# Kernel tuning notes

Hardware: AMD Instinct MI355X
Metric: run time of the kernel (lower is better)

## Reference

```python
import jax, jax.numpy as jnp
import numpy as np

HEADS = 12
KEY_DIM = 16
B, C, H, W = 16, 384, 64, 64


def _hard_swish(x):
    return x * jnp.clip(x + 3.0, 0.0, 6.0) / 6.0


def _affine(x, g, b):
    # Inference-mode BatchNorm folded into per-channel scale/shift (NCHW).
    return x * g[:, None, None] + b[:, None, None]


def _pw(x, w):
    # 1x1 conv as a channel contraction: x [B,Cin,H,W], w [Cout,Cin].
    return jnp.einsum('bchw,oc->bohw', x, w)


def setup_inputs() -> dict:
    key = jax.random.key(0)
    ks = jax.random.split(key, 20)
    d = {}
    d['x'] = jax.random.normal(ks[0], (B, C, H, W), dtype=jnp.float32)
    d['rnd_offset'] = jax.random.uniform(ks[1], (B, 2, 1, 1), dtype=jnp.float32) * 6.0 - 3.0
    S = HEADS * KEY_DIM  # 192
    d['proj_w'] = jax.random.normal(ks[2], (3 * S, C + 2), dtype=jnp.float32) * 0.05
    d['proj_g'] = jax.random.uniform(ks[3], (3 * S,), dtype=jnp.float32) + 0.5
    d['proj_b'] = jax.random.normal(ks[4], (3 * S,), dtype=jnp.float32) * 0.1
    d['vp2_w'] = jax.random.normal(ks[5], (C, S), dtype=jnp.float32) * 0.05
    d['vp2_g'] = jax.random.uniform(ks[6], (C,), dtype=jnp.float32) + 0.5
    d['vp2_b'] = jax.random.normal(ks[7], (C,), dtype=jnp.float32) * 0.1
    d['dw_w'] = jax.random.normal(ks[8], (C, 1, 5, 5), dtype=jnp.float32) * 0.1
    d['dw_g'] = jax.random.uniform(ks[9], (C,), dtype=jnp.float32) + 0.5
    d['dw_b'] = jax.random.normal(ks[10], (C,), dtype=jnp.float32) * 0.1
    d['pw1_w'] = jax.random.normal(ks[11], (4 * C, C), dtype=jnp.float32) * 0.05
    d['pw1_g'] = jax.random.uniform(ks[12], (4 * C,), dtype=jnp.float32) + 0.5
    d['pw1_b'] = jax.random.normal(ks[13], (4 * C,), dtype=jnp.float32) * 0.1
    d['pw2_w'] = jax.random.normal(ks[14], (C, 4 * C), dtype=jnp.float32) * 0.05
    d['out_g'] = jax.random.uniform(ks[15], (C,), dtype=jnp.float32) + 0.5
    d['out_b'] = jax.random.normal(ks[16], (C,), dtype=jnp.float32) * 0.1
    d['rz_attn'] = jnp.float32(0.1)
    d['rz_ffn'] = jnp.float32(0.1)
    d['embed_strength'] = jnp.float32(-10.0)
    return d


def reference(x, rnd_offset, proj_w, proj_g, proj_b, vp2_w, vp2_g, vp2_b,
              dw_w, dw_g, dw_b, pw1_w, pw1_g, pw1_b, pw2_w, out_g, out_b,
              rz_attn, rz_ffn, embed_strength):
    b, c, h, w = x.shape
    # --- learned-strength positional embedding with random per-image offset ---
    xp = jnp.arange(w, dtype=x.dtype) / 1000.0
    yp = jnp.arange(h, dtype=x.dtype) / 1000.0
    xx, yy = jnp.meshgrid(xp, yp, indexing='xy')      # each (H, W)
    pos = jnp.stack([xx, yy], axis=0)[None]           # (1, 2, H, W)
    pos = jnp.exp(embed_strength) * (pos + rnd_offset)  # (B, 2, H, W)
    x_emb = jnp.concatenate([x, pos], axis=1)         # (B, C+2, H, W)

    # --- qkv projection (1x1 conv + BN + ReLU), computed in fp32 ---
    proj = jax.nn.relu(_affine(_pw(x_emb, proj_w), proj_g, proj_b))
    proj = proj.astype(jnp.float32)

    S = HEADS * KEY_DIM
    N = h * w

    def get_slice(i):
        # (B, S, H, W) slice -> (B*heads, N, key_dim)
        s = proj[:, i * S:(i + 1) * S]
        return s.reshape(b * HEADS, KEY_DIM, N).transpose(0, 2, 1)

    q, k, v = get_slice(0), get_slice(1), get_slice(2)

    # --- non-causal linear attention: Q (K^T V) / (Q sum(K)) ---
    ktv = jnp.einsum('bnd,bne->bde', k, v)            # (B*heads, d, d)
    numer = jnp.einsum('bnd,bde->bne', q, ktv)        # (B*heads, N, d)
    denom = jnp.einsum('bnd,bd->bn', q, k.sum(axis=1))[..., None]  # (B*heads, N, 1)
    out = numer / jnp.maximum(denom, 1e-4)
    out = out.transpose(0, 2, 1).reshape(b, S, h, w)  # (B, heads*key_dim, H, W)

    # --- value projection back to channels ---
    out = jax.nn.relu(_affine(_pw(out, vp2_w), vp2_g, vp2_b))
    y = x + rz_attn * out

    # --- FFN: depthwise 5x5 -> expand 1x1 -> project 1x1 (+ BNs) ---
    z = jax.lax.conv_general_dilated(
        y, dw_w, window_strides=(1, 1), padding='SAME',
        dimension_numbers=('NCHW', 'OIHW', 'NCHW'), feature_group_count=c)
    z = _hard_swish(_affine(z, dw_g, dw_b))
    z = _hard_swish(_affine(_pw(z, pw1_w), pw1_g, pw1_b))
    z = _affine(_pw(z, pw2_w), out_g, out_b)
    return y + rz_ffn * z
```

## Files before the change

### kernel.cpp

```cpp
#include <hip/hip_runtime.h>
#include <cstdint>

typedef unsigned short u16;
typedef __attribute__((ext_vector_type(8))) __bf16 bf16x8;
typedef __attribute__((ext_vector_type(4))) float f32x4;

__device__ __forceinline__ u16 f2bf(float f) {
    union { float f; uint32_t u; } v; v.f = f;
    uint32_t u = v.u;
    uint32_t r = (u + 0x7fffu + ((u >> 16) & 1u)) >> 16;
    return (u16)r;
}
__device__ __forceinline__ float bf2f(u16 h) {
    union { uint32_t u; float f; } v; v.u = ((uint32_t)h) << 16;
    return v.f;
}
__device__ __forceinline__ float bflo(uint32_t u) {
    union { uint32_t u; float f; } v; v.u = u << 16;
    return v.f;
}
__device__ __forceinline__ float bfhi(uint32_t u) {
    union { uint32_t u; float f; } v; v.u = u & 0xffff0000u;
    return v.f;
}

__device__ __forceinline__ void ld_lds16(const u16* g, u16* l) {
    __builtin_amdgcn_global_load_lds(
        (const __attribute__((address_space(1))) uint32_t*)g,
        (__attribute__((address_space(3))) uint32_t*)l, 16, 0, 0);
}

__global__ __launch_bounds__(256) void prep(
    const float* __restrict__ proj_w, const float* __restrict__ proj_g,
    const float* __restrict__ proj_b, const float* __restrict__ vp2_w,
    const float* __restrict__ pw1_w, const float* __restrict__ pw2_w,
    const float* __restrict__ dw_w,
    u16* __restrict__ w1p, u16* __restrict__ w2, u16* __restrict__ w3,
    u16* __restrict__ w4, float* __restrict__ gp, float2* __restrict__ dwp)
{
    int i = blockIdx.x * 256 + threadIdx.x;
    if (i < 245760) {
        int o = i / 384, k = i - o * 384;
        w1p[i] = (o < 576) ? f2bf(proj_w[o * 386 + k]) : (u16)0;
        return;
    }
    i -= 245760;
    if (i < 73728) { w2[i] = f2bf(vp2_w[i]); return; }
    i -= 73728;
    if (i < 589824) { w3[i] = f2bf(pw1_w[i]); return; }
    i -= 589824;
    if (i < 589824) { w4[i] = f2bf(pw2_w[i]); return; }
    i -= 589824;
    if (i < 2560) {
        int which = i / 640, o = i - which * 640;
        float v = 0.f;
        if (o < 576) {
            v = (which == 0) ? proj_g[o] : (which == 1) ? proj_b[o]
                : (which == 2) ? proj_w[o * 386 + 384] : proj_w[o * 386 + 385];
        }
        gp[i] = v; return;
    }
    i -= 2560;
    if (i < 4800) {
        int tap = i / 192, cp = i - tap * 192;
        dwp[i] = make_float2(dw_w[(2 * cp) * 25 + tap], dw_w[(2 * cp + 1) * 25 + tap]);
    }
}

__global__ __launch_bounds__(256) void transpose_x(const float* __restrict__ x,
                                                   u16* __restrict__ xt)
{
    __shared__ float tile[64][65];
    int b = blockIdx.x, n0 = blockIdx.y * 64, c0 = blockIdx.z * 64;
    int t = threadIdx.x;
    int jj = t & 63, i0 = t >> 6;
    #pragma unroll
    for (int r = 0; r < 16; r++) {
        int ci = r * 4 + i0;
        tile[ci][jj] = x[((size_t)b * 384 + c0 + ci) * 4096 + n0 + jj];
    }
    __syncthreads();
    #pragma unroll
    for (int r = 0; r < 16; r++) {
        int ni = r * 4 + i0;
        xt[(size_t)(b * 4096 + n0 + ni) * 384 + c0 + jj] = f2bf(tile[jj][ni]);
    }
}

template <int MODE, int IM, int JN, int OUTT>
__global__ __launch_bounds__(256) void gemm_nhwc(
    const u16* __restrict__ A, const u16* __restrict__ W,
    u16* __restrict__ out, int K, int Osz, int nOT,
    const float* __restrict__ g, const float* __restrict__ bb,
    const float* __restrict__ w1x, const float* __restrict__ w1y,
    const u16* __restrict__ res, const float* __restrict__ sc,
    const float* __restrict__ rnd)
{
    constexpr int BK = 32;
    constexpr int BM = IM * 32;
    constexpr int BN = JN * 32;
    constexpr int GA = IM / 2;
    constexpr int GB = JN / 2;
    constexpr bool LEGACY = (IM == 4 && JN == 4);
    constexpr bool SPB = (JN >= IM);
    constexpr int NBUF = LEGACY ? 3 : 2;
    constexpr int NP1 = LEGACY ? 0 : (SPB ? GB / 2 : GA / 2);
    constexpr int NP0 = LEGACY ? 0 : (GA + GB - NP1);
    __shared__ __align__(16) u16 smem[NBUF * (BM + BN) * BK];

    const int tid = threadIdx.x;
    const int lane = tid & 63;
    const int wv = tid >> 6;
    const int wm = (wv >> 1) * (IM * 16);
    const int wn = (wv & 1) * (JN * 16);

    const int nwg = gridDim.x;
    const int q8 = nwg >> 3;
    const int b1 = (blockIdx.x & 7) * q8 + (blockIdx.x >> 3);
    const int mt = b1 / nOT;
    const int ot = b1 - mt * nOT;
    const int m0 = mt * BM;
    const int o0 = ot * BN;

    const int q = lane >> 4;
    const int mr = lane & 15;
    const int ks = (q ^ ((mr >> 1) & 3)) * 8;

    const int tq = tid >> 2;
    const int sl = tid & 3;
    const int tk = (sl ^ ((tq >> 1) & 3)) * 8;

    size_t ga[GA], gb[GB];
    int la[GA], lb[GB];
    #pragma unroll
    for (int gi = 0; gi < GA; gi++) {
        ga[gi] = (size_t)(m0 + gi * 64 + tq) * K + tk;
        la[gi] = (gi * 64 + tq) * BK + sl * 8;
    }
    #pragma unroll
    for (int gi = 0; gi < GB; gi++) {
        gb[gi] = (size_t)(o0 + gi * 64 + tq) * K + tk;
        lb[gi] = (gi * 64 + tq) * BK + sl * 8;
    }

    auto stage_all = [&](int tile, int bufi) {
        const size_t ko = (size_t)tile * BK;
        u16* sAb = smem + bufi * (BM * BK);
        u16* sBb = smem + NBUF * (BM * BK) + bufi * (BN * BK);
        #pragma unroll
        for (int gi = 0; gi < GA; gi++) ld_lds16(A + ga[gi] + ko, sAb + la[gi]);
        #pragma unroll
        for (int gi = 0; gi < GB; gi++) ld_lds16(W + gb[gi] + ko, sBb + lb[gi]);
    };
    auto stage_s0 = [&](int tile, int bufi) {
        const size_t ko = (size_t)tile * BK;
        u16* sAb = smem + bufi * (BM * BK);
        u16* sBb = smem + NBUF * (BM * BK) + bufi * (BN * BK);
        if constexpr (SPB) {
            #pragma unroll
            for (int gi = 0; gi < GA; gi++) ld_lds16(A + ga[gi] + ko, sAb + la[gi]);
            #pragma unroll
            for (int gi = 0; gi < GB; gi += 2) ld_lds16(W + gb[gi] + ko, sBb + lb[gi]);
        } else {
            #pragma unroll
            for (int gi = 0; gi < GA; gi += 2) ld_lds16(A + ga[gi] + ko, sAb + la[gi]);
            #pragma unroll
            for (int gi = 0; gi < GB; gi++) ld_lds16(W + gb[gi] + ko, sBb + lb[gi]);
        }
    };
    auto stage_s1 = [&](int tile, int bufi) {
        const size_t ko = (size_t)tile * BK;
        u16* sAb = smem + bufi * (BM * BK);
        u16* sBb = smem + NBUF * (BM * BK) + bufi * (BN * BK);
        if constexpr (SPB) {
            #pragma unroll
            for (int gi = 1; gi < GB; gi += 2) ld_lds16(W + gb[gi] + ko, sBb + lb[gi]);
        } else {
            #pragma unroll
            for (int gi = 1; gi < GA; gi += 2) ld_lds16(A + ga[gi] + ko, sAb + la[gi]);
        }
    };

    f32x4 acc[IM][JN] = {};
    const int nIter = K >> 5;
    int buf = 0;

    if constexpr (LEGACY) {
        stage_all(0, 0);
        if (nIter > 1) stage_all(1, 1);
        for (int t = 0; t < nIter; ++t) {
            if (t + 1 < nIter) asm volatile("s_waitcnt vmcnt(4)" ::: "memory");
            else               asm volatile("s_waitcnt vmcnt(0)" ::: "memory");
            __builtin_amdgcn_s_barrier();
            __builtin_amdgcn_sched_barrier(0);
            if (t + 2 < nIter) {
                int nb = buf + 2; if (nb >= 3) nb -= 3;
                stage_all(t + 2, nb);
            }
            const u16* sAr = smem + buf * (BM * BK);
            const u16* sBr = smem + NBUF * (BM * BK) + buf * (BN * BK);
            bf16x8 af[IM], bfr[JN];
            #pragma unroll
            for (int i = 0; i < IM; i++)
                af[i] = *(const bf16x8*)&sAr[(wm + i * 16 + mr) * BK + ks];
            #pragma unroll
            for (int j = 0; j < JN; j++)
                bfr[j] = *(const bf16x8*)&sBr[(wn + j * 16 + mr) * BK + ks];
            __builtin_amdgcn_s_setprio(1);
            #pragma unroll
            for (int i = 0; i < IM; i++)
                #pragma unroll
                for (int j = 0; j < JN; j++)
                    acc[i][j] = __builtin_amdgcn_mfma_f32_16x16x32_bf16(af[i], bfr[j], acc[i][j], 0, 0, 0);
            __builtin_amdgcn_s_setprio(0);
            buf++; if (buf == 3) buf = 0;
        }
    } else {
        stage_s0(0, 0);
        stage_s1(0, 0);
        for (int t = 0; t < nIter; ++t) {
            const u16* sAr = smem + buf * (BM * BK);
            const u16* sBr = smem + NBUF * (BM * BK) + buf * (BN * BK);
            bf16x8 af[IM], bfr[JN];
            asm volatile("s_waitcnt vmcnt(%0)" ::"i"(NP1) : "memory");
            __builtin_amdgcn_s_barrier();
            __builtin_amdgcn_sched_barrier(0);
            if constexpr (SPB) {
                #pragma unroll
                for (int i = 0; i < IM; i++)
                    af[i] = *(const bf16x8*)&sAr[(wm + i * 16 + mr) * BK + ks];
                #pragma unroll
                for (int j = 0; j < JN / 2; j++)
                    bfr[j] = *(const bf16x8*)&sBr[(wn + j * 16 + mr) * BK + ks];
            } else {
                #pragma unroll
                for (int i = 0; i < IM / 2; i++)
                    af[i] = *(const bf16x8*)&sAr[(wm + i * 16 + mr) * BK + ks];
                #pragma unroll
                for (int j = 0; j < JN; j++)
                    bfr[j] = *(const bf16x8*)&sBr[(wn + j * 16 + mr) * BK + ks];
            }
            if (t + 1 < nIter) stage_s0(t + 1, buf ^ 1);
            __builtin_amdgcn_s_setprio(1);
            if constexpr (SPB) {
                #pragma unroll
                for (int i = 0; i < IM; i++)
                    #pragma unroll
                    for (int j = 0; j < JN / 2; j++)
                        acc[i][j] = __builtin_amdgcn_mfma_f32_16x16x32_bf16(af[i], bfr[j], acc[i][j], 0, 0, 0);
            } else {
                #pragma unroll
                for (int i = 0; i < IM / 2; i++)
                    #pragma unroll
                    for (int j = 0; j < JN; j++)
                        acc[i][j] = __builtin_amdgcn_mfma_f32_16x16x32_bf16(af[i], bfr[j], acc[i][j], 0, 0, 0);
            }
            __builtin_amdgcn_s_setprio(0);
            if (t + 1 < nIter)
                asm volatile("s_waitcnt vmcnt(%0)" ::"i"(NP0) : "memory");
            else
                asm volatile("s_waitcnt vmcnt(0)" ::: "memory");
            __builtin_amdgcn_s_barrier();
            __builtin_amdgcn_sched_barrier(0);
            if constexpr (SPB) {
                #pragma unroll
                for (int j = JN / 2; j < JN; j++)
                    bfr[j] = *(const bf16x8*)&sBr[(wn + j * 16 + mr) * BK + ks];
            } else {
                #pragma unroll
                for (int i = IM / 2; i < IM; i++)
                    af[i] = *(const bf16x8*)&sAr[(wm + i * 16 + mr) * BK + ks];
            }
            if (t + 1 < nIter) stage_s1(t + 1, buf ^ 1);
            __builtin_amdgcn_s_setprio(1);
            if constexpr (SPB) {
                #pragma unroll
                for (int i = 0; i < IM; i++)
                    #pragma unroll
                    for (int j = JN / 2; j < JN; j++)
                        acc[i][j] = __builtin_amdgcn_mfma_f32_16x16x32_bf16(af[i], bfr[j], acc[i][j], 0, 0, 0);
            } else {
                #pragma unroll
                for (int i = IM / 2; i < IM; i++)
                    #pragma unroll
                    for (int j = 0; j < JN; j++)
                        acc[i][j] = __builtin_amdgcn_mfma_f32_16x16x32_bf16(af[i], bfr[j], acc[i][j], 0, 0, 0);
            }
            __builtin_amdgcn_s_setprio(0);
            buf ^= 1;
        }
    }

    float* st = (float*)smem;
    constexpr int LDE = BN + 4;
    constexpr int P = BM / 32;
    constexpr int HP = IM / 2;
    constexpr int NG = BN / 128;
    const int row_l = tid >> 3;
    const int cs16 = (tid & 7) * 16;

    float E = 0.f, offx = 0.f, offy = 0.f, rz = 0.f;
    if constexpr (MODE == 1) {
        E = expf(sc[0]);
        int bimg = m0 >> 12;
        offx = rnd[bimg * 2 + 0];
        offy = rnd[bimg * 2 + 1];
    }
    if constexpr (MODE == 2 || MODE == 4) rz = sc[0];

    float gv[NG][16], bv[NG][16];
    #pragma unroll
    for (int gg = 0; gg < NG; gg++)
        #pragma unroll
        for (int c = 0; c < 4; c++) {
            *(float4*)&gv[gg][c * 4] = *(const float4*)(g + o0 + gg * 128 + cs16 + c * 4);
            *(float4*)&bv[gg][c * 4] = *(const float4*)(bb + o0 + gg * 128 + cs16 + c * 4);
        }
    float wxv[16], wyv[16];
    if constexpr (MODE == 1) {
        #pragma unroll
        for (int c = 0; c < 4; c++) {
            *(float4*)&wxv[c * 4] = *(const float4*)(w1x + o0 + cs16 + c * 4);
            *(float4*)&wyv[c * 4] = *(const float4*)(w1y + o0 + cs16 + c * 4);
        }
    }

    #pragma unroll
    for (int p = 0; p < P; ++p) {
        __syncthreads();
        if ((wv >> 1) == p / HP) {
            const int ib = (p % HP) * 2;
            #pragma unroll
            for (int ii = 0; ii < 2; ++ii)
                #pragma unroll
                for (int j = 0; j < JN; ++j)
                    #pragma unroll
                    for (int r = 0; r < 4; ++r)
                        st[(ii * 16 + q * 4 + r) * LDE + wn + j * 16 + mr] =
                            acc[ib + ii][j][r];
        }
        __syncthreads();
        const int pix = m0 + p * 32 + row_l;
        float px = 0.f, py = 0.f;
        if constexpr (MODE == 1) {
            int n = pix & 4095;
            px = E * ((float)(n & 63) * 0.001f + offx);
            py = E * ((float)(n >> 6) * 0.001f + offy);
        }
        #pragma unroll
        for (int gg = 0; gg < NG; ++gg) {
            const int ob = o0 + gg * 128 + cs16;
            float vals[16];
            #pragma unroll
            for (int c = 0; c < 4; ++c)
                *(f32x4*)&vals[c * 4] =
                    *(const f32x4*)&st[row_l * LDE + gg * 128 + cs16 + c * 4];
            u16 rv[16];
            if constexpr (MODE == 2 || MODE == 4) {
                #pragma unroll
                for (int c = 0; c < 2; c++)
                    *(float4*)&rv[c * 8] = *(const float4*)(res + (size_t)pix * 384 + ob + c * 8);
            }
            float fv[16];
            #pragma unroll
            for (int e = 0; e < 16; ++e) {
                float v = vals[e];
                if constexpr (MODE == 1) {
                    v += px * wxv[e] + py * wyv[e];
                    v = fmaxf(gv[gg][e] * v + bv[gg][e], 0.f);
                } else if constexpr (MODE == 2) {
                    v = fmaxf(gv[gg][e] * v + bv[gg][e], 0.f);
                    v = bf2f(rv[e]) + rz * v;
                } else if constexpr (MODE == 3) {
                    float tv = gv[gg][e] * v + bv[gg][e];
                    v = tv * fminf(fmaxf(tv + 3.f, 0.f), 6.f) * (1.f / 6.f);
                } else {
                    float tv = gv[gg][e] * v + bv[gg][e];
                    v = bf2f(rv[e]) + rz * tv;
                }
                fv[e] = v;
            }
            if constexpr (OUTT) {
                #pragma unroll
                for (int c = 0; c < 4; ++c)
                    *(f32x4*)&st[row_l * LDE + gg * 128 + cs16 + c * 4] =
                        *(const f32x4*)&fv[c * 4];
            } else {
                u16 ov[16];
                #pragma unroll
                for (int e = 0; e < 16; ++e) ov[e] = f2bf(fv[e]);
                #pragma unroll
                for (int c = 0; c < 2; c++)
                    *(float4*)(out + (size_t)pix * Osz + ob + c * 8) = *(const float4*)&ov[c * 8];
            }
        }
        if constexpr (OUTT) {
            __syncthreads();
            const int cl = tid & 127;
            const int rh = tid >> 7;
            const int pixb = m0 + p * 32;
            const int bimg2 = pixb >> 12;
            const int n0 = (pixb & 4095) + rh * 16;
            float tv[16];
            #pragma unroll
            for (int k2 = 0; k2 < 16; ++k2)
                tv[k2] = st[(rh * 16 + k2) * LDE + cl];
            float* dst = (float*)out + ((size_t)bimg2 * 384 + o0 + cl) * 4096 + n0;
            #pragma unroll
            for (int c = 0; c < 4; c++)
                *(float4*)(dst + c * 4) = *(const float4*)&tv[c * 4];
        }
    }
}

__global__ __launch_bounds__(256) void attn_ktv(const u16* __restrict__ proj,
                                                float* __restrict__ ktvp)
{
    constexpr int LDT = 264;
    __shared__ u16 kt_[16 * LDT];
    __shared__ u16 vt_[16 * LDT];
    int bh = blockIdx.x;
    int ch = blockIdx.y;
    int b = bh / 12, h = bh - b * 12;
    const u16* base = proj + (size_t)b * 4096 * 640;
    int kc = 192 + h * 16, vc = 384 + h * 16;
    int t = threadIdx.x;
    int d = t >> 4, e = t & 15;
    float acc = 0.f, ksum = 0.f;
    for (int n0 = ch * 1024; n0 < ch * 1024 + 1024; n0 += 256) {
        __syncthreads();
        const u16* r = base + (size_t)(n0 + t) * 640;
        u16 kv[16], vv[16];
        *(float4*)&kv[0] = ((const float4*)(r + kc))[0];
        *(float4*)&kv[8] = ((const float4*)(r + kc))[1];
        *(float4*)&vv[0] = ((const float4*)(r + vc))[0];
        *(float4*)&vv[8] = ((const float4*)(r + vc))[1];
        #pragma unroll
        for (int dd = 0; dd < 16; dd++) {
            kt_[dd * LDT + t] = kv[dd];
            vt_[dd * LDT + t] = vv[dd];
        }
        __syncthreads();
        const u16* kr = &kt_[d * LDT];
        const u16* vr = &vt_[e * LDT];
        #pragma unroll 4
        for (int n = 0; n < 256; n += 8) {
            uint4 kw = *(const uint4*)(kr + n);
            uint4 vw = *(const uint4*)(vr + n);
            acc += bflo(kw.x) * bflo(vw.x) + bfhi(kw.x) * bfhi(vw.x);
            acc += bflo(kw.y) * bflo(vw.y) + bfhi(kw.y) * bfhi(vw.y);
            acc += bflo(kw.z) * bflo(vw.z) + bfhi(kw.z) * bfhi(vw.z);
            acc += bflo(kw.w) * bflo(vw.w) + bfhi(kw.w) * bfhi(vw.w);
        }
        if (t < 16) {
            const u16* krs = &kt_[t * LDT];
            #pragma unroll 4
            for (int n = 0; n < 256; n += 8) {
                uint4 kw = *(const uint4*)(krs + n);
                ksum += bflo(kw.x) + bfhi(kw.x) + bflo(kw.y) + bfhi(kw.y)
                      + bflo(kw.z) + bfhi(kw.z) + bflo(kw.w) + bfhi(kw.w);
            }
        }
    }
    float* o = ktvp + ((size_t)bh * 4 + ch) * 272;
    o[t] = acc;
    if (t < 16) o[256 + t] = ksum;
}

__global__ __launch_bounds__(256) void attn_apply(const u16* __restrict__ proj,
                                                  const float* __restrict__ ktvp,
                                                  u16* __restrict__ att)
{
    int bh = blockIdx.x;
    int b = bh / 12, h = bh - b * 12;
    __shared__ float kt[272];
    int t = threadIdx.x;
    {
        const float* p = ktvp + (size_t)bh * 4 * 272;
        kt[t] = p[t] + p[272 + t] + p[544 + t] + p[816 + t];
        if (t < 16) {
            int u = 256 + t;
            kt[u] = p[u] + p[272 + u] + p[544 + u] + p[816 + u];
        }
    }
    __syncthreads();
    int n = blockIdx.y * 256 + t;
    const u16* qr = proj + (size_t)(b * 4096 + n) * 640 + h * 16;
    u16 qb[16];
    *(float4*)&qb[0] = ((const float4*)qr)[0];
    *(float4*)&qb[8] = ((const float4*)qr)[1];
    float qv[16];
    #pragma unroll
    for (int d = 0; d < 16; d++) qv[d] = bf2f(qb[d]);
    float denom = 0.f;
    #pragma unroll
    for (int d = 0; d < 16; d++) denom += qv[d] * kt[256 + d];
    float rcp = 1.f / fmaxf(denom, 1e-4f);
    u16* op = att + (size_t)(b * 4096 + n) * 192 + h * 16;
    u16 ov[16];
    #pragma unroll
    for (int e = 0; e < 16; e++) {
        float s = 0.f;
        #pragma unroll
        for (int d = 0; d < 16; d++) s += qv[d] * kt[d * 16 + e];
        ov[e] = f2bf(s * rcp);
    }
    ((float4*)op)[0] = *(const float4*)&ov[0];
    ((float4*)op)[1] = *(const float4*)&ov[8];
}

__global__ __launch_bounds__(192) void dwconv(const u16* __restrict__ y,
                                              const float2* __restrict__ wt,
                                              const float* __restrict__ g,
                                              const float* __restrict__ bc,
                                              u16* __restrict__ z)
{
    const int cp = threadIdx.x;
    const int xc = blockIdx.x;
    const int b  = blockIdx.y;
    const int c0 = cp * 2;

    float2 wv[25];
    #pragma unroll
    for (int t = 0; t < 25; t++) wv[t] = wt[t * 192 + cp];
    const float g0 = g[c0], g1 = g[c0 + 1];
    const float b0 = bc[c0], b1 = bc[c0 + 1];

    const size_t ibase = (size_t)b * 4096;
    const u16* ycol = y + ibase * 384 + c0;

    uint32_t r0[5], r1[5], r2[5], r3[5], r4[5];

#define LOADROW(yy, dst)                                                     \
    {                                                                        \
        if ((unsigned)(yy) < 64u) {                                          \
            const u16* rp = ycol + (size_t)(yy) * 64 * 384;                  \
            _Pragma("unroll")                                                \
            for (int dx = 0; dx < 5; dx++) {                                 \
                int xx = xc + dx - 2;                                        \
                dst[dx] = ((unsigned)xx < 64u)                               \
                              ? *(const uint32_t*)(rp + (size_t)xx * 384)    \
                              : 0u;                                          \
            }                                                                \
        } else {                                                             \
            _Pragma("unroll")                                                \
            for (int dx = 0; dx < 5; dx++) dst[dx] = 0u;                     \
        }                                                                    \
    }

#define COMPUTE(yr, A, B, C, D, E)                                           \
    if ((yr) < 64) {                                                         \
        float a0 = 0.f, a1 = 0.f;                                            \
        _Pragma("unroll")                                                    \
        for (int dx = 0; dx < 5; dx++) {                                     \
            uint32_t p;                                                      \
            p = A[dx];                                                       \
            a0 += wv[dx].x * bf2f((u16)(p & 0xffffu));                       \
            a1 += wv[dx].y * bf2f((u16)(p >> 16));                           \
            p = B[dx];                                                       \
            a0 += wv[5 + dx].x * bf2f((u16)(p & 0xffffu));                   \
            a1 += wv[5 + dx].y * bf2f((u16)(p >> 16));                       \
            p = C[dx];                                                       \
            a0 += wv[10 + dx].x * bf2f((u16)(p & 0xffffu));                  \
            a1 += wv[10 + dx].y * bf2f((u16)(p >> 16));                      \
            p = D[dx];                                                       \
            a0 += wv[15 + dx].x * bf2f((u16)(p & 0xffffu));                  \
            a1 += wv[15 + dx].y * bf2f((u16)(p >> 16));                      \
            p = E[dx];                                                       \
            a0 += wv[20 + dx].x * bf2f((u16)(p & 0xffffu));                  \
            a1 += wv[20 + dx].y * bf2f((u16)(p >> 16));                      \
        }                                                                    \
        float t0 = g0 * a0 + b0;                                             \
        float t1 = g1 * a1 + b1;                                             \
        t0 = t0 * fminf(fmaxf(t0 + 3.f, 0.f), 6.f) * (1.f / 6.f);            \
        t1 = t1 * fminf(fmaxf(t1 + 3.f, 0.f), 6.f) * (1.f / 6.f);            \
        uint32_t packed = (uint32_t)f2bf(t0) | ((uint32_t)f2bf(t1) << 16);   \
        *(uint32_t*)(z + (ibase + (size_t)(yr) * 64 + xc) * 384 + c0) = packed; \
    }

#define STEP(yr, A, B, C, D, E)                                              \
    COMPUTE(yr, A, B, C, D, E)                                               \
    LOADROW((yr) + 3, A)

    LOADROW(-2, r0)
    LOADROW(-1, r1)
    LOADROW(0, r2)
    LOADROW(1, r3)
    LOADROW(2, r4)

    for (int base = 0; base < 65; base += 5) {
        STEP(base + 0, r0, r1, r2, r3, r4)
        STEP(base + 1, r1, r2, r3, r4, r0)
        STEP(base + 2, r2, r3, r4, r0, r1)
        STEP(base + 3, r3, r4, r0, r1, r2)
        STEP(base + 4, r4, r0, r1, r2, r3)
    }
#undef STEP
#undef COMPUTE
#undef LOADROW
}

extern "C" void kernel_launch(void* const* d_in, const int* in_sizes, int n_in,
                              void* d_out, int out_size, void* d_ws, size_t ws_size,
                              hipStream_t stream)
{
    (void)in_sizes; (void)n_in; (void)out_size; (void)ws_size;
    const float* x       = (const float*)d_in[0];
    const float* rnd     = (const float*)d_in[1];
    const float* proj_w  = (const float*)d_in[2];
    const float* proj_g  = (const float*)d_in[3];
    const float* proj_b  = (const float*)d_in[4];
    const float* vp2_w   = (const float*)d_in[5];
    const float* vp2_g   = (const float*)d_in[6];
    const float* vp2_b   = (const float*)d_in[7];
    const float* dw_w    = (const float*)d_in[8];
    const float* dw_g    = (const float*)d_in[9];
    const float* dw_b    = (const float*)d_in[10];
    const float* pw1_w   = (const float*)d_in[11];
    const float* pw1_g   = (const float*)d_in[12];
    const float* pw1_b   = (const float*)d_in[13];
    const float* pw2_w   = (const float*)d_in[14];
    const float* out_g   = (const float*)d_in[15];
    const float* out_b   = (const float*)d_in[16];
    const float* rz_attn = (const float*)d_in[17];
    const float* rz_ffn  = (const float*)d_in[18];
    const float* es      = (const float*)d_in[19];
    float* out = (float*)d_out;

    char* ws = (char*)d_ws;
    u16*   xt   = (u16*)(ws + 0);
    u16*   att  = (u16*)(ws + 50331648);
    u16*   z2   = (u16*)(ws + 0);
    u16*   proj = (u16*)(ws + 201326592);
    u16*   z1   = proj;
    u16*   yt   = (u16*)(ws + 285212672);
    u16*   w1p  = (u16*)(ws + 335753216);
    u16*   w2   = (u16*)(ws + 336244736);
    u16*   w3   = (u16*)(ws + 336392192);
    u16*   w4   = (u16*)(ws + 337571840);
    float* gp   = (float*)(ws + 338751488);
    float2* dwp = (float2*)(ws + 338761728);
    float* ktvp = (float*)(ws + 338800128);

    prep<<<5885, 256, 0, stream>>>(proj_w, proj_g, proj_b, vp2_w, pw1_w, pw2_w,
                                   dw_w, w1p, w2, w3, w4, gp, dwp);
    transpose_x<<<dim3(16, 64, 6), 256, 0, stream>>>(x, xt);
    gemm_nhwc<1, 4, 4, 0><<<2560, 256, 0, stream>>>(xt, w1p, proj, 384, 640, 5,
        gp, gp + 640, gp + 1280, gp + 1920, nullptr, es, rnd);
    attn_ktv<<<dim3(192, 4), 256, 0, stream>>>(proj, ktvp);
    attn_apply<<<dim3(192, 16), 256, 0, stream>>>(proj, ktvp, att);
    gemm_nhwc<2, 8, 4, 0><<<768, 256, 0, stream>>>(att, w2, yt, 192, 384, 3,
        vp2_g, vp2_b, nullptr, nullptr, xt, rz_attn, nullptr);
    dwconv<<<dim3(64, 16), 192, 0, stream>>>(yt, dwp, dw_g, dw_b, z1);
    gemm_nhwc<3, 4, 8, 0><<<3072, 256, 0, stream>>>(z1, w3, z2, 384, 1536, 6,
        pw1_g, pw1_b, nullptr, nullptr, nullptr, nullptr, nullptr);
    gemm_nhwc<4, 8, 4, 1><<<768, 256, 0, stream>>>(z2, w4, (u16*)out, 1536, 384, 3,
        out_g, out_b, nullptr, nullptr, yt, rz_ffn, nullptr);
}
```

Before: 666.4 us.

## Fuse FFN expand and project GEMMs into one kernel keeping hidden tile on-chip

Replaces the two FFN pointwise GEMM launches with a single kernel. Each 64-pixel block computes the 1536-wide hidden activation in 256-column chunks, applies BN and hard-swish, stages the chunk in LDS, and immediately accumulates it into the 384-channel output. This removes the round trip of the large z2 intermediate through HBM. In exchange the block holds 24 accumulator vectors in registers, uses about 94KB of LDS, and has fewer blocks per CU, which may lower occupancy.

```diff
diff --git a/kernel.cpp b/kernel.cpp
--- a/kernel.cpp
+++ b/kernel.cpp
@@ -406,6 +406,215 @@
             for (int k2 = 0; k2 < 16; ++k2)
                 tv[k2] = st[(rh * 16 + k2) * LDE + cl];
             float* dst = (float*)out + ((size_t)bimg2 * 384 + o0 + cl) * 4096 + n0;
+            #pragma unroll
+            for (int c = 0; c < 4; c++)
+                *(float4*)(dst + c * 4) = *(const float4*)&tv[c * 4];
+        }
+    }
+}
+
+__global__ __launch_bounds__(256) void ffn_fused(
+    const u16* __restrict__ z1, const u16* __restrict__ W3,
+    const u16* __restrict__ W4, const u16* __restrict__ res,
+    const float* __restrict__ g1, const float* __restrict__ b1f,
+    const float* __restrict__ g2, const float* __restrict__ b2f,
+    const float* __restrict__ sc, float* __restrict__ outp)
+{
+    __shared__ __align__(16) u16 smem[47104];
+    u16* sA = smem;
+    u16* sB = smem + 6144;
+    u16* sS = smem + 30720;
+
+    const int tid = threadIdx.x;
+    const int lane = tid & 63, wv = tid >> 6;
+    const int q = lane >> 4, mr = lane & 15;
+    const int wm1 = (wv >> 1) * 32;
+    const int wn1 = (wv & 1) * 128;
+    const int ks = (q ^ ((mr >> 1) & 3)) * 8;
+
+    const int nwg = gridDim.x;
+    const int q8 = nwg >> 3;
+    const int bsw = (blockIdx.x & 7) * q8 + (blockIdx.x >> 3);
+    const int m0 = bsw * 64;
+
+    const int tq = tid >> 2, sl = tid & 3;
+    const int tk = (sl ^ ((tq >> 1) & 3)) * 8;
+    const int loA = tid * 8;
+
+    const size_t gaA = (size_t)(m0 + tq) * 384 + tk;
+
+    const int R2 = wv * 16 + mr;
+    const int sbz = (q ^ ((R2 >> 1) & 3)) * 8;
+
+    f32x4 acc2[24] = {};
+
+    for (int ot = 0; ot < 6; ++ot) {
+        f32x4 acc1[2][8] = {};
+        const size_t w3b = (size_t)(ot * 256 + tq) * 384 + tk;
+        ld_lds16(z1 + gaA, sA + loA);
+        #pragma unroll
+        for (int gi = 0; gi < 4; gi++)
+            ld_lds16(W3 + w3b + (size_t)gi * 24576, sB + gi * 2048 + loA);
+        ld_lds16(z1 + gaA + 32, sA + 2048 + loA);
+        #pragma unroll
+        for (int gi = 0; gi < 4; gi++)
+            ld_lds16(W3 + w3b + 32 + (size_t)gi * 24576, sB + 8192 + gi * 2048 + loA);
+        int buf = 0;
+        for (int t = 0; t < 12; ++t) {
+            if (t < 11) asm volatile("s_waitcnt vmcnt(5)" ::: "memory");
+            else        asm volatile("s_waitcnt vmcnt(0)" ::: "memory");
+            __builtin_amdgcn_s_barrier();
+            __builtin_amdgcn_sched_barrier(0);
+            if (t + 2 < 12) {
+                int nb = buf + 2; if (nb >= 3) nb -= 3;
+                const int ko = (t + 2) * 32;
+                ld_lds16(z1 + gaA + ko, sA + nb * 2048 + loA);
+                #pragma unroll
+                for (int gi = 0; gi < 4; gi++)
+                    ld_lds16(W3 + w3b + ko + (size_t)gi * 24576,
+                             sB + nb * 8192 + gi * 2048 + loA);
+            }
+            const u16* sAr = sA + buf * 2048;
+            const u16* sBr = sB + buf * 8192;
+            bf16x8 af[2], bfr[8];
+            #pragma unroll
+            for (int i = 0; i < 2; i++)
+                af[i] = *(const bf16x8*)&sAr[(wm1 + i * 16 + mr) * 32 + ks];
+            #pragma unroll
+            for (int j = 0; j < 8; j++)
+                bfr[j] = *(const bf16x8*)&sBr[(wn1 + j * 16 + mr) * 32 + ks];
+            __builtin_amdgcn_s_setprio(1);
+            #pragma unroll
+            for (int i = 0; i < 2; i++)
+                #pragma unroll
+                for (int j = 0; j < 8; j++)
+                    acc1[i][j] = __builtin_amdgcn_mfma_f32_16x16x32_bf16(af[i], bfr[j], acc1[i][j], 0, 0, 0);
+            __builtin_amdgcn_s_setprio(0);
+            buf++; if (buf == 3) buf = 0;
+        }
+        float g3v[8], b3v[8];
+        #pragma unroll
+        for (int j = 0; j < 8; ++j) {
+            const int col = ot * 256 + wn1 + j * 16 + mr;
+            g3v[j] = g1[col]; b3v[j] = b1f[col];
+        }
+        #pragma unroll
+        for (int i = 0; i < 2; ++i)
+            #pragma unroll
+            for (int j = 0; j < 8; ++j) {
+                const int colL = wn1 + j * 16 + mr;
+                #pragma unroll
+                for (int r = 0; r < 4; ++r) {
+                    const int row1 = wm1 + i * 16 + q * 4 + r;
+                    float tv = g3v[j] * acc1[i][j][r] + b3v[j];
+                    float hv = tv * fminf(fmaxf(tv + 3.f, 0.f), 6.f) * (1.f / 6.f);
+                    const int slot = ((colL >> 3) & 3) ^ ((row1 >> 1) & 3);
+                    sS[row1 * 256 + (colL >> 5) * 32 + slot * 8 + (colL & 7)] = f2bf(hv);
+                }
+            }
+        __syncthreads();
+        bf16x8 z2r[8];
+        #pragma unroll
+        for (int kk = 0; kk < 8; ++kk)
+            z2r[kk] = *(const bf16x8*)&sS[R2 * 256 + kk * 32 + sbz];
+        asm volatile("s_waitcnt lgkmcnt(0)" ::: "memory");
+        __builtin_amdgcn_sched_barrier(0);
+        const int t2b = ot * 8;
+        #pragma unroll
+        for (int gi = 0; gi < 6; gi++)
+            ld_lds16(W4 + (size_t)(gi * 64 + tq) * 1536 + t2b * 32 + tk,
+                     smem + gi * 2048 + loA);
+        #pragma unroll
+        for (int gi = 0; gi < 6; gi++)
+            ld_lds16(W4 + (size_t)(gi * 64 + tq) * 1536 + (t2b + 1) * 32 + tk,
+                     smem + 12288 + gi * 2048 + loA);
+        #pragma unroll
+        for (int kk = 0; kk < 8; ++kk) {
+            if (kk < 7) asm volatile("s_waitcnt vmcnt(6)" ::: "memory");
+            else        asm volatile("s_waitcnt vmcnt(0)" ::: "memory");
+            __builtin_amdgcn_s_barrier();
+            __builtin_amdgcn_sched_barrier(0);
+            if (kk + 2 < 8) {
+                const int nb = (kk + 2) % 3;
+                #pragma unroll
+                for (int gi = 0; gi < 6; gi++)
+                    ld_lds16(W4 + (size_t)(gi * 64 + tq) * 1536 + (t2b + kk + 2) * 32 + tk,
+                             smem + nb * 12288 + gi * 2048 + loA);
+            }
+            const u16* sW = smem + (kk % 3) * 12288;
+            bf16x8 bfr2[12];
+            #pragma unroll
+            for (int j = 0; j < 12; j++)
+                bfr2[j] = *(const bf16x8*)&sW[(j * 16 + mr) * 32 + ks];
+            __builtin_amdgcn_s_setprio(1);
+            #pragma unroll
+            for (int j = 0; j < 12; j++)
+                acc2[j] = __builtin_amdgcn_mfma_f32_16x16x32_bf16(z2r[kk], bfr2[j], acc2[j], 0, 0, 0);
+            __builtin_amdgcn_s_setprio(0);
+            #pragma unroll
+            for (int j = 0; j < 12; j++)
+                bfr2[j] = *(const bf16x8*)&sW[((j + 12) * 16 + mr) * 32 + ks];
+            __builtin_amdgcn_s_setprio(1);
+            #pragma unroll
+            for (int j = 0; j < 12; j++)
+                acc2[12 + j] = __builtin_amdgcn_mfma_f32_16x16x32_bf16(z2r[kk], bfr2[j], acc2[12 + j], 0, 0, 0);
+            __builtin_amdgcn_s_setprio(0);
+        }
+        __syncthreads();
+    }
+    const float rz = sc[0];
+    float* stE = (float*)smem;
+    const int row_l = tid >> 3;
+    const int cs16 = (tid & 7) * 16;
+    float gv[3][16], bv[3][16];
+    #pragma unroll
+    for (int gg = 0; gg < 3; gg++)
+        #pragma unroll
+        for (int c = 0; c < 4; c++) {
+            *(float4*)&gv[gg][c * 4] = *(const float4*)(g2 + gg * 128 + cs16 + c * 4);
+            *(float4*)&bv[gg][c * 4] = *(const float4*)(b2f + gg * 128 + cs16 + c * 4);
+        }
+    const int cl = tid & 127, rh = tid >> 7;
+    const int bimg = m0 >> 12;
+    #pragma unroll
+    for (int s = 0; s < 2; ++s) {
+        __syncthreads();
+        if ((wv >> 1) == s) {
+            #pragma unroll
+            for (int j = 0; j < 24; ++j)
+                #pragma unroll
+                for (int r = 0; r < 4; ++r)
+                    stE[((wv & 1) * 16 + q * 4 + r) * 388 + j * 16 + mr] = acc2[j][r];
+        }
+        __syncthreads();
+        const int pix = m0 + s * 32 + row_l;
+        #pragma unroll
+        for (int gg = 0; gg < 3; ++gg) {
+            float vals[16];
+            #pragma unroll
+            for (int c = 0; c < 4; ++c)
+                *(f32x4*)&vals[c * 4] = *(const f32x4*)&stE[row_l * 388 + gg * 128 + cs16 + c * 4];
+            u16 rv[16];
+            #pragma unroll
+            for (int c = 0; c < 2; c++)
+                *(float4*)&rv[c * 8] = *(const float4*)(res + (size_t)pix * 384 + gg * 128 + cs16 + c * 8);
+            float fv[16];
+            #pragma unroll
+            for (int e = 0; e < 16; ++e)
+                fv[e] = bf2f(rv[e]) + rz * (gv[gg][e] * vals[e] + bv[gg][e]);
+            #pragma unroll
+            for (int c = 0; c < 4; ++c)
+                *(f32x4*)&stE[row_l * 388 + gg * 128 + cs16 + c * 4] = *(const f32x4*)&fv[c * 4];
+        }
+        __syncthreads();
+        const int n0 = (m0 & 4095) + s * 32 + rh * 16;
+        #pragma unroll
+        for (int gc = 0; gc < 3; ++gc) {
+            float tv[16];
+            #pragma unroll
+            for (int k2 = 0; k2 < 16; ++k2)
+                tv[k2] = stE[(rh * 16 + k2) * 388 + gc * 128 + cl];
+            float* dst = outp + ((size_t)bimg * 384 + gc * 128 + cl) * 4096 + n0;
             #pragma unroll
             for (int c = 0; c < 4; c++)
                 *(float4*)(dst + c * 4) = *(const float4*)&tv[c * 4];
@@ -630,7 +839,6 @@
     char* ws = (char*)d_ws;
     u16*   xt   = (u16*)(ws + 0);
     u16*   att  = (u16*)(ws + 50331648);
-    u16*   z2   = (u16*)(ws + 0);
     u16*   proj = (u16*)(ws + 201326592);
     u16*   z1   = proj;
     u16*   yt   = (u16*)(ws + 285212672);
@@ -652,8 +860,6 @@
     gemm_nhwc<2, 8, 4, 0><<<768, 256, 0, stream>>>(att, w2, yt, 192, 384, 3,
         vp2_g, vp2_b, nullptr, nullptr, xt, rz_attn, nullptr);
     dwconv<<<dim3(64, 16), 192, 0, stream>>>(yt, dwp, dw_g, dw_b, z1);
-    gemm_nhwc<3, 4, 8, 0><<<3072, 256, 0, stream>>>(z1, w3, z2, 384, 1536, 6,
-        pw1_g, pw1_b, nullptr, nullptr, nullptr, nullptr, nullptr);
-    gemm_nhwc<4, 8, 4, 1><<<768, 256, 0, stream>>>(z2, w4, (u16*)out, 1536, 384, 3,
-        out_g, out_b, nullptr, nullptr, yt, rz_ffn, nullptr);
-}
+    ffn_fused<<<1024, 256, 0, stream>>>(z1, w3, w4, yt, pw1_g, pw1_b,
+        out_g, out_b, rz_ffn, out);
+}
```

Measured after the change: 734.5 us. 1.1x slower.
